# Optimization experiments

Measured on AMD Instinct MI355X. Metric: run time of the kernel, lower is better.

The kernel has to match this reference:

```python
import jax, jax.numpy as jnp
import numpy as np

N = 50000      # nodes
E = 800000     # edges (avg degree 16)
IN = 512       # input features
OUT = 32       # per-head hidden features
H = 8          # heads (layer 1)
C = 16         # classes (layer 2, 1 head)
NEG_SLOPE = 0.2


def setup_inputs() -> dict:
    key = jax.random.key(0)
    ks = jax.random.split(key, 8)
    x = jax.random.normal(ks[0], (N, IN), jnp.float32)
    edge_index = jax.random.randint(ks[1], (2, E), 0, N, jnp.int32)
    # layer 1 params: W1 [IN, H*OUT], attention vectors a1_src/a1_dst [H, OUT]
    W1 = jax.random.normal(ks[2], (IN, H * OUT), jnp.float32) * (1.0 / np.sqrt(IN))
    a1_src = jax.random.normal(ks[3], (H, OUT), jnp.float32) * (1.0 / np.sqrt(OUT))
    a1_dst = jax.random.normal(ks[4], (H, OUT), jnp.float32) * (1.0 / np.sqrt(OUT))
    # layer 2 params: single head, W2 [H*OUT, C], a2_src/a2_dst [1, C]
    W2 = jax.random.normal(ks[5], (H * OUT, C), jnp.float32) * (1.0 / np.sqrt(H * OUT))
    a2_src = jax.random.normal(ks[6], (1, C), jnp.float32) * (1.0 / np.sqrt(C))
    a2_dst = jax.random.normal(ks[7], (1, C), jnp.float32) * (1.0 / np.sqrt(C))
    return {"x": x, "W1": W1, "a1_src": a1_src, "a1_dst": a1_dst,
            "W2": W2, "a2_src": a2_src, "a2_dst": a2_dst,
            "edge_index": edge_index}


def gat_layer(x, edge_index, W, a_src, a_dst, concat):
    """Standard GAT layer: e_ij = LeakyReLU(a_src.Wh_i + a_dst.Wh_j),
    softmax over incoming edges of each target node, scatter-aggregate."""
    n = x.shape[0]
    h_heads, f = a_src.shape
    h = (x @ W).reshape(n, h_heads, f)                      # [N, H, F]
    src, dst = edge_index[0], edge_index[1]
    es = jnp.einsum('nhf,hf->nh', h, a_src)                 # [N, H] per-node src scores
    ed = jnp.einsum('nhf,hf->nh', h, a_dst)                 # [N, H]
    e = jax.nn.leaky_relu(es[src] + ed[dst], NEG_SLOPE)     # [E, H] per-edge logits
    # segment softmax over edges grouped by dst node
    m = jax.ops.segment_max(e, dst, num_segments=n)         # [N, H]
    m = jnp.where(jnp.isfinite(m), m, 0.0)                  # empty segments -> -inf
    p = jnp.exp(e - m[dst])                                 # [E, H]
    s = jax.ops.segment_sum(p, dst, num_segments=n)         # [N, H]
    denom = s[dst]
    alpha = p / jnp.where(denom > 0, denom, 1.0)            # [E, H]
    msg = h[src] * alpha[:, :, None]                        # [E, H, F]
    out = jax.ops.segment_sum(msg, dst, num_segments=n)     # [N, H, F]
    if concat:
        return out.reshape(n, h_heads * f)
    return out.mean(axis=1)


def reference(x, W1, a1_src, a1_dst, W2, a2_src, a2_dst, edge_index):
    # dropout is identity in eval mode
    h = gat_layer(x, edge_index, W1, a1_src, a1_dst, concat=True)   # [N, H*OUT]
    h = jax.nn.elu(h)
    h = gat_layer(h, edge_index, W2, a2_src, a2_dst, concat=False)  # [N, C]
    return jax.nn.log_softmax(h, axis=1)
```

## Files before the change

kernel.cpp:

```cpp
#include <hip/hip_runtime.h>

#define NN 50000
#define EE 800000
#define KIN 512
#define HF 256
#define NH 8
#define FOUT 32
#define NC 16
#define NEG 0.2f
#define NB_SCAN 196

typedef unsigned short u16;
typedef __attribute__((ext_vector_type(8))) short shortx8;
typedef __attribute__((ext_vector_type(4))) float floatx4;
typedef __attribute__((ext_vector_type(8))) unsigned short ushortx8;
typedef __attribute__((ext_vector_type(4))) unsigned short ushortx4;

__device__ __forceinline__ float lrelu(float x) { return x > 0.f ? x : NEG * x; }

__device__ __forceinline__ u16 f2bf(float f) {
    unsigned u = __float_as_uint(f);
    return (u16)((u + 0x7FFFu + ((u >> 16) & 1u)) >> 16);
}
__device__ __forceinline__ float bf2f(u16 v) {
    return __uint_as_float((unsigned)v << 16);
}

__device__ __forceinline__ void gll16(const void* g, void* l) {
    __builtin_amdgcn_global_load_lds((const __attribute__((address_space(1))) void*)g,
                                     (__attribute__((address_space(3))) void*)l, 16, 0, 0);
}

__global__ void count_deg(const int* __restrict__ dst, int* __restrict__ deg) {
    int e = blockIdx.x * 256 + threadIdx.x;
    if (e < EE) atomicAdd(&deg[dst[e]], 1);
}

__global__ __launch_bounds__(256) void scan_a(const int* __restrict__ deg, int* __restrict__ bsum) {
    __shared__ int sm[256];
    int t = threadIdx.x;
    int i = blockIdx.x * 256 + t;
    sm[t] = (i < NN) ? deg[i] : 0;
    __syncthreads();
    for (int o = 128; o; o >>= 1) { if (t < o) sm[t] += sm[t + o]; __syncthreads(); }
    if (t == 0) bsum[blockIdx.x] = sm[0];
}

__global__ __launch_bounds__(256) void scan_b(const int* __restrict__ bsum, int* __restrict__ boff) {
    __shared__ int sm[256];
    int t = threadIdx.x;
    sm[t] = (t < NB_SCAN) ? bsum[t] : 0;
    __syncthreads();
    for (int d = 1; d < 256; d <<= 1) {
        int v = (t >= d) ? sm[t - d] : 0;
        __syncthreads();
        sm[t] += v;
        __syncthreads();
    }
    if (t < NB_SCAN) boff[t] = (t == 0) ? 0 : sm[t - 1];
}

__global__ __launch_bounds__(256) void scan_c(const int* __restrict__ deg, const int* __restrict__ boff,
                                              int* __restrict__ off) {
    __shared__ int sm[256];
    int t = threadIdx.x;
    int i = blockIdx.x * 256 + t;
    int d = (i < NN) ? deg[i] : 0;
    sm[t] = d;
    __syncthreads();
    for (int dd = 1; dd < 256; dd <<= 1) {
        int v = (t >= dd) ? sm[t - dd] : 0;
        __syncthreads();
        sm[t] += v;
        __syncthreads();
    }
    if (i < NN) off[i] = boff[blockIdx.x] + sm[t] - d;
    if (i == 0) off[NN] = EE;
}

__global__ void fill_csr(const int* __restrict__ src, const int* __restrict__ dst,
                         const int* __restrict__ off, int* __restrict__ cursor,
                         int* __restrict__ csr_src) {
    int e = blockIdx.x * 256 + threadIdx.x;
    if (e < EE) {
        int d = dst[e];
        int pos = atomicAdd(&cursor[d], 1);
        csr_src[off[d] + pos] = src[e];
    }
}

__global__ __launch_bounds__(256) void convert_x(const float* __restrict__ x, u16* __restrict__ xb) {
    size_t i = ((size_t)blockIdx.x * 256 + threadIdx.x) * 8;
    if (i >= (size_t)NN * KIN) return;
    float4 f0 = *(const float4*)(x + i);
    float4 f1 = *(const float4*)(x + i + 4);
    ushortx8 o;
    o[0] = f2bf(f0.x); o[1] = f2bf(f0.y); o[2] = f2bf(f0.z); o[3] = f2bf(f0.w);
    o[4] = f2bf(f1.x); o[5] = f2bf(f1.y); o[6] = f2bf(f1.z); o[7] = f2bf(f1.w);
    *(ushortx8*)(xb + i) = o;
}

__global__ __launch_bounds__(256) void convert_w1t(const float* __restrict__ W1, u16* __restrict__ w1t) {
    int e = blockIdx.x * 256 + threadIdx.x;
    int k = e >> 8, n = e & 255;
    w1t[n * KIN + k] = f2bf(W1[e]);
}

__global__ __launch_bounds__(256) void convert_w2t(const float* __restrict__ W2, u16* __restrict__ w2t) {
    int e = blockIdx.x * 256 + threadIdx.x;
    int k = e >> 4, c = e & 15;
    w2t[c * HF + k] = f2bf(W2[e]);
}

__global__ __launch_bounds__(256) void gemm1_mfma(const u16* __restrict__ xb,
                                                  const u16* __restrict__ w1t,
                                                  u16* __restrict__ h1b) {
    __shared__ __align__(16) u16 As[128 * 32];
    __shared__ __align__(16) u16 Bs[128 * 32];
    int t = threadIdx.x;
    int lane = t & 63, wave = t >> 6;
    int wm = wave >> 1, wn = wave & 1;
    int lm = lane & 15, quad = lane >> 4;
    int bm = blockIdx.x * 128;
    int bn = blockIdx.y * 128;

    floatx4 acc[4][4];
#pragma unroll
    for (int i = 0; i < 4; i++)
#pragma unroll
        for (int j = 0; j < 4; j++) acc[i][j] = (floatx4){0.f, 0.f, 0.f, 0.f};

    int sr = wave * 32 + (lane >> 2);
    int sk = (lane & 3) * 8;
    int ar0 = bm + sr, ar1 = ar0 + 16;
    if (ar0 > NN - 1) ar0 = NN - 1;
    if (ar1 > NN - 1) ar1 = NN - 1;
    const u16* agp0 = xb + (size_t)ar0 * KIN + sk;
    const u16* agp1 = xb + (size_t)ar1 * KIN + sk;
    const u16* bgp0 = w1t + (size_t)(bn + sr) * KIN + sk;
    const u16* bgp1 = w1t + (size_t)(bn + sr + 16) * KIN + sk;
    u16* asl0 = As + wave * 1024;
    u16* asl1 = As + wave * 1024 + 512;
    u16* bsl0 = Bs + wave * 1024;
    u16* bsl1 = Bs + wave * 1024 + 512;

    int offA[4], offB[4];
#pragma unroll
    for (int i = 0; i < 4; i++) offA[i] = (wm * 64 + i * 16 + lm) * 32 + quad * 8;
#pragma unroll
    for (int j = 0; j < 4; j++) offB[j] = (wn * 64 + j * 16 + lm) * 32 + quad * 8;

    for (int kk = 0; kk < KIN; kk += 32) {
        gll16(agp0 + kk, asl0);
        gll16(agp1 + kk, asl1);
        gll16(bgp0 + kk, bsl0);
        gll16(bgp1 + kk, bsl1);
        __syncthreads();
        shortx8 af[4], bf[4];
#pragma unroll
        for (int i = 0; i < 4; i++) af[i] = *(const shortx8*)&As[offA[i]];
#pragma unroll
        for (int j = 0; j < 4; j++) bf[j] = *(const shortx8*)&Bs[offB[j]];
#pragma unroll
        for (int i = 0; i < 4; i++)
#pragma unroll
            for (int j = 0; j < 4; j++)
                acc[i][j] = __builtin_amdgcn_mfma_f32_16x16x32_bf16(af[i], bf[j], acc[i][j], 0, 0, 0);
        __syncthreads();
    }

#pragma unroll
    for (int i = 0; i < 4; i++) {
        int row = bm + wm * 64 + i * 16 + quad * 4;
#pragma unroll
        for (int j = 0; j < 4; j++) {
            int col = bn + wn * 64 + j * 16 + lm;
#pragma unroll
            for (int r = 0; r < 4; r++) {
                if (row + r < NN) h1b[(size_t)(row + r) * HF + col] = f2bf(acc[i][j][r]);
            }
        }
    }
}

__global__ __launch_bounds__(256) void scores1(const u16* __restrict__ h1b, const float* __restrict__ a_src,
                                               const float* __restrict__ a_dst,
                                               float* __restrict__ es, float* __restrict__ ed) {
    __shared__ float as_s[HF], ad_s[HF];
    int t = threadIdx.x;
    as_s[t] = a_src[t];
    ad_s[t] = a_dst[t];
    __syncthreads();
    int nl = t >> 5;
    int L = t & 31;
    int n = blockIdx.x * 8 + nl;
    ushortx8 hv = *(const ushortx8*)(h1b + (size_t)n * HF + L * 8);
    float ps = 0.f, pd = 0.f;
#pragma unroll
    for (int i = 0; i < 8; i++) {
        float v = bf2f(hv[i]);
        ps += v * as_s[L * 8 + i];
        pd += v * ad_s[L * 8 + i];
    }
    ps += __shfl_down(ps, 2, 4); ps += __shfl_down(ps, 1, 4);
    pd += __shfl_down(pd, 2, 4); pd += __shfl_down(pd, 1, 4);
    if ((L & 3) == 0) {
        int h = L >> 2;
        es[n * NH + h] = ps;
        ed[n * NH + h] = pd;
    }
}

__global__ __launch_bounds__(256) void agg1(const u16* __restrict__ h1b, const float* __restrict__ es,
                                            const float* __restrict__ ed, const int* __restrict__ off,
                                            const int* __restrict__ csr_src, u16* __restrict__ out1b) {
    int n = blockIdx.x, t = threadIdx.x;
    __shared__ float edl[NH];
    __shared__ float p_chunk[32][9];
    __shared__ float s_h[NH];
    __shared__ int src_chunk[32];
    __shared__ float red[4][HF];
    int beg = off[n];
    int deg = off[n + 1] - beg;
    if (t < NH) edl[t] = ed[n * NH + t];
    int ph = t >> 5, el = t & 31;
    int w = t >> 6, L = t & 63;
    int ah = L >> 3;
    float s_part = 0.f;
    float acc0 = 0.f, acc1 = 0.f, acc2 = 0.f, acc3 = 0.f;
    __syncthreads();
    float edh = edl[ph];
    for (int base = 0; base < deg; base += 32) {
        int nch = deg - base; if (nch > 32) nch = 32;
        if (t < nch) src_chunk[t] = csr_src[beg + base + t];
        __syncthreads();
        ushortx4 hv[8];
#pragma unroll
        for (int i = 0; i < 8; i++) {
            int e = w + i * 4;
            if (e < nch) hv[i] = *(const ushortx4*)(h1b + (size_t)src_chunk[e] * HF + L * 4);
        }
        float p = 0.f;
        if (el < nch) p = __expf(lrelu(es[src_chunk[el] * NH + ph] + edh));
        s_part += p;
        p_chunk[el][ph] = p;
        __syncthreads();
#pragma unroll
        for (int i = 0; i < 8; i++) {
            int e = w + i * 4;
            if (e < nch) {
                float p2 = p_chunk[e][ah];
                acc0 += p2 * bf2f(hv[i][0]);
                acc1 += p2 * bf2f(hv[i][1]);
                acc2 += p2 * bf2f(hv[i][2]);
                acc3 += p2 * bf2f(hv[i][3]);
            }
        }
        __syncthreads();
    }
#pragma unroll
    for (int o = 16; o; o >>= 1) s_part += __shfl_down(s_part, o, 32);
    if (el == 0) s_h[ph] = s_part;
    *(float4*)&red[w][L * 4] = make_float4(acc0, acc1, acc2, acc3);
    __syncthreads();
    float vv = red[0][t] + red[1][t] + red[2][t] + red[3][t];
    float sh = s_h[t >> 5];
    vv *= (sh > 0.f ? 1.0f / sh : 0.f);
    out1b[(size_t)n * HF + t] = f2bf(vv > 0.f ? vv : (__expf(vv) - 1.0f));
}

__global__ __launch_bounds__(64) void gemm2_mfma(const u16* __restrict__ out1b, const u16* __restrict__ w2t,
                                                 const float* __restrict__ a2s, const float* __restrict__ a2d,
                                                 float* __restrict__ h2, float* __restrict__ es2,
                                                 float* __restrict__ ed2) {
    int lane = threadIdx.x;
    int lm = lane & 15, quad = lane >> 4;
    int nb = blockIdx.x * 16;
    floatx4 acc = (floatx4){0.f, 0.f, 0.f, 0.f};
    const u16* arow = out1b + (size_t)(nb + lm) * HF + quad * 8;
    const u16* brow = w2t + lm * HF + quad * 8;
#pragma unroll
    for (int kk = 0; kk < HF; kk += 32) {
        shortx8 af = *(const shortx8*)(arow + kk);
        shortx8 bf = *(const shortx8*)(brow + kk);
        acc = __builtin_amdgcn_mfma_f32_16x16x32_bf16(af, bf, acc, 0, 0, 0);
    }
    float a2sc = a2s[lm], a2dc = a2d[lm];
#pragma unroll
    for (int r = 0; r < 4; r++) {
        int n = nb + quad * 4 + r;
        float v = acc[r];
        h2[n * NC + lm] = v;
        float ps = v * a2sc, pd = v * a2dc;
#pragma unroll
        for (int o = 8; o; o >>= 1) {
            ps += __shfl_down(ps, o, 16);
            pd += __shfl_down(pd, o, 16);
        }
        if (lm == 0) { es2[n] = ps; ed2[n] = pd; }
    }
}

__global__ __launch_bounds__(256) void agg2(const float* __restrict__ h2, const float* __restrict__ es2,
                                            const float* __restrict__ ed2, const int* __restrict__ off,
                                            const int* __restrict__ csr_src, float* __restrict__ out) {
    int t = threadIdx.x;
    int nid = blockIdx.x * 16 + (t >> 4);
    int c = t & 15;
    int beg = off[nid];
    int deg = off[nid + 1] - beg;
    float edn = ed2[nid];
    float s = 0.f, acc = 0.f;
    for (int base = 0; base < deg; base += 16) {
        int nch = deg - base; if (nch > 16) nch = 16;
        int sv = 0;
        if (c < nch) sv = csr_src[beg + base + c];
        int sva[16];
#pragma unroll
        for (int e = 0; e < 16; e++) sva[e] = __shfl(sv, e, 16);
        float hva[16];
#pragma unroll
        for (int e = 0; e < 16; e++) hva[e] = h2[sva[e] * NC + c];
        float p = 0.f;
        if (c < nch) p = __expf(lrelu(es2[sv] + edn));
        s += p;
        float pa[16];
#pragma unroll
        for (int e = 0; e < 16; e++) pa[e] = __shfl(p, e, 16);
#pragma unroll
        for (int e = 0; e < 16; e++) acc += pa[e] * hva[e];
    }
#pragma unroll
    for (int o = 8; o; o >>= 1) s += __shfl_down(s, o, 16);
    s = __shfl(s, 0, 16);
    float v = (s > 0.f) ? acc / s : 0.f;
    float m2 = v;
#pragma unroll
    for (int o = 8; o; o >>= 1) m2 = fmaxf(m2, __shfl_down(m2, o, 16));
    m2 = __shfl(m2, 0, 16);
    float se = __expf(v - m2);
#pragma unroll
    for (int o = 8; o; o >>= 1) se += __shfl_down(se, o, 16);
    se = __shfl(se, 0, 16);
    out[nid * NC + c] = v - m2 - __logf(se);
}

extern "C" void kernel_launch(void* const* d_in, const int* in_sizes, int n_in,
                              void* d_out, int out_size, void* d_ws, size_t ws_size,
                              hipStream_t stream) {
    const float* x   = (const float*)d_in[0];
    const float* W1  = (const float*)d_in[1];
    const float* a1s = (const float*)d_in[2];
    const float* a1d = (const float*)d_in[3];
    const float* W2  = (const float*)d_in[4];
    const float* a2s = (const float*)d_in[5];
    const float* a2d = (const float*)d_in[6];
    const int*   ei  = (const int*)d_in[7];
    const int* srcv = ei;
    const int* dstv = ei + EE;
    float* out = (float*)d_out;

    u16* h1b   = (u16*)d_ws;
    u16* xb    = h1b + (size_t)NN * HF;
    u16* out1b = xb;
    float* es1 = (float*)(xb + (size_t)NN * KIN);
    float* ed1 = es1 + (size_t)NN * NH;
    float* h2  = ed1 + (size_t)NN * NH;
    u16* w1t   = (u16*)h2;
    float* es2v = h2 + (size_t)NN * NC;
    float* ed2v = es2v + NN;
    int* deg    = (int*)(ed2v + NN);
    int* cursor = deg + NN;
    int* offs   = cursor + NN;
    int* csr    = offs + NN + 1;
    int* bsum   = csr + EE;
    int* boff   = bsum + 256;
    u16* w2t    = (u16*)(boff + 256);

    hipMemsetAsync(deg, 0, NN * sizeof(int), stream);
    hipMemsetAsync(cursor, 0, NN * sizeof(int), stream);
    count_deg<<<(EE + 255) / 256, 256, 0, stream>>>(dstv, deg);
    scan_a<<<NB_SCAN, 256, 0, stream>>>(deg, bsum);
    scan_b<<<1, 256, 0, stream>>>(bsum, boff);
    scan_c<<<NB_SCAN, 256, 0, stream>>>(deg, boff, offs);
    fill_csr<<<(EE + 255) / 256, 256, 0, stream>>>(srcv, dstv, offs, cursor, csr);
    convert_x<<<((size_t)NN * KIN / 8 + 255) / 256, 256, 0, stream>>>(x, xb);
    convert_w1t<<<(KIN * HF) / 256, 256, 0, stream>>>(W1, w1t);
    convert_w2t<<<(HF * NC) / 256, 256, 0, stream>>>(W2, w2t);
    gemm1_mfma<<<dim3((NN + 127) / 128, HF / 128), 256, 0, stream>>>(xb, w1t, h1b);
    scores1<<<NN / 8, 256, 0, stream>>>(h1b, a1s, a1d, es1, ed1);
    agg1<<<NN, 256, 0, stream>>>(h1b, es1, ed1, offs, csr, out1b);
    gemm2_mfma<<<NN / 16, 64, 0, stream>>>(out1b, w2t, a2s, a2d, h2, es2v, ed2v);
    agg2<<<NN / 16, 256, 0, stream>>>(h2, es2v, ed2v, offs, csr, out);
}
```

Baseline: 424.6 us.

## Fuse fp32-to-bf16 x conversion into GEMM1, widen N tile, wave-per-node aggregation

GEMM1 now loads fp32 x directly into LDS and converts to bf16 while building fragments. This removes the separate convert_x pass and its 50000x512 bf16 round trip through memory. Each block now covers all 256 output columns, so x is read once instead of twice, at the cost of more accumulator registers and more LDS. agg1 is rewritten to process one node per wave with no __syncthreads and vectorized 16-byte feature loads. The weight conversions and the two memsets are each merged into one launch.

```diff
diff --git a/kernel.cpp b/kernel.cpp
--- a/kernel.cpp
+++ b/kernel.cpp
@@ -14,7 +14,7 @@
 typedef __attribute__((ext_vector_type(8))) short shortx8;
 typedef __attribute__((ext_vector_type(4))) float floatx4;
 typedef __attribute__((ext_vector_type(8))) unsigned short ushortx8;
-typedef __attribute__((ext_vector_type(4))) unsigned short ushortx4;
+typedef __attribute__((ext_vector_type(4))) unsigned uintx4;
 
 __device__ __forceinline__ float lrelu(float x) { return x > 0.f ? x : NEG * x; }
 
@@ -24,6 +24,10 @@
 }
 __device__ __forceinline__ float bf2f(u16 v) {
     return __uint_as_float((unsigned)v << 16);
+}
+__device__ __forceinline__ unsigned pk2bf(float a, float b) {
+    unsigned ua = __float_as_uint(a), ub = __float_as_uint(b);
+    return ((ua + 0x8000u) >> 16) | ((ub + 0x8000u) & 0xffff0000u);
 }
 
 __device__ __forceinline__ void gll16(const void* g, void* l) {
@@ -89,82 +93,90 @@
     }
 }
 
-__global__ __launch_bounds__(256) void convert_x(const float* __restrict__ x, u16* __restrict__ xb) {
-    size_t i = ((size_t)blockIdx.x * 256 + threadIdx.x) * 8;
-    if (i >= (size_t)NN * KIN) return;
-    float4 f0 = *(const float4*)(x + i);
-    float4 f1 = *(const float4*)(x + i + 4);
-    ushortx8 o;
-    o[0] = f2bf(f0.x); o[1] = f2bf(f0.y); o[2] = f2bf(f0.z); o[3] = f2bf(f0.w);
-    o[4] = f2bf(f1.x); o[5] = f2bf(f1.y); o[6] = f2bf(f1.z); o[7] = f2bf(f1.w);
-    *(ushortx8*)(xb + i) = o;
-}
-
-__global__ __launch_bounds__(256) void convert_w1t(const float* __restrict__ W1, u16* __restrict__ w1t) {
+__global__ __launch_bounds__(256) void convert_w(const float* __restrict__ W1, const float* __restrict__ W2,
+                                                 u16* __restrict__ w1t, u16* __restrict__ w2t) {
     int e = blockIdx.x * 256 + threadIdx.x;
-    int k = e >> 8, n = e & 255;
-    w1t[n * KIN + k] = f2bf(W1[e]);
-}
-
-__global__ __launch_bounds__(256) void convert_w2t(const float* __restrict__ W2, u16* __restrict__ w2t) {
-    int e = blockIdx.x * 256 + threadIdx.x;
-    int k = e >> 4, c = e & 15;
-    w2t[c * HF + k] = f2bf(W2[e]);
-}
-
-__global__ __launch_bounds__(256) void gemm1_mfma(const u16* __restrict__ xb,
-                                                  const u16* __restrict__ w1t,
-                                                  u16* __restrict__ h1b) {
-    __shared__ __align__(16) u16 As[128 * 32];
-    __shared__ __align__(16) u16 Bs[128 * 32];
+    if (e < KIN * HF) {
+        int k = e >> 8, n = e & 255;
+        w1t[n * KIN + k] = f2bf(W1[e]);
+    } else {
+        int e2 = e - KIN * HF;
+        if (e2 < HF * NC) {
+            int k = e2 >> 4, c = e2 & 15;
+            w2t[c * HF + k] = f2bf(W2[e2]);
+        }
+    }
+}
+
+__global__ __launch_bounds__(256, 2) void gemm1_mfma(const float* __restrict__ x,
+                                                     const u16* __restrict__ w1t,
+                                                     u16* __restrict__ h1b) {
+    __shared__ __align__(16) float As[128 * 32];
+    __shared__ __align__(16) u16 Bs[256 * 32];
     int t = threadIdx.x;
     int lane = t & 63, wave = t >> 6;
     int wm = wave >> 1, wn = wave & 1;
     int lm = lane & 15, quad = lane >> 4;
     int bm = blockIdx.x * 128;
-    int bn = blockIdx.y * 128;
-
-    floatx4 acc[4][4];
+
+    floatx4 acc[4][8];
 #pragma unroll
     for (int i = 0; i < 4; i++)
 #pragma unroll
-        for (int j = 0; j < 4; j++) acc[i][j] = (floatx4){0.f, 0.f, 0.f, 0.f};
-
-    int sr = wave * 32 + (lane >> 2);
-    int sk = (lane & 3) * 8;
-    int ar0 = bm + sr, ar1 = ar0 + 16;
-    if (ar0 > NN - 1) ar0 = NN - 1;
-    if (ar1 > NN - 1) ar1 = NN - 1;
-    const u16* agp0 = xb + (size_t)ar0 * KIN + sk;
-    const u16* agp1 = xb + (size_t)ar1 * KIN + sk;
-    const u16* bgp0 = w1t + (size_t)(bn + sr) * KIN + sk;
-    const u16* bgp1 = w1t + (size_t)(bn + sr + 16) * KIN + sk;
-    u16* asl0 = As + wave * 1024;
-    u16* asl1 = As + wave * 1024 + 512;
-    u16* bsl0 = Bs + wave * 1024;
-    u16* bsl1 = Bs + wave * 1024 + 512;
-
-    int offA[4], offB[4];
+        for (int j = 0; j < 8; j++) acc[i][j] = (floatx4){0.f, 0.f, 0.f, 0.f};
+
+    int arow_l = wave * 32 + (lane >> 3);
+    int akoff = (lane & 7) * 4;
+    const float* aptr[4];
+#pragma unroll
+    for (int i = 0; i < 4; i++) {
+        int ar = bm + arow_l + i * 8;
+        if (ar > NN - 1) ar = NN - 1;
+        aptr[i] = x + (size_t)ar * KIN + akoff;
+    }
+    float* alds[4];
+#pragma unroll
+    for (int i = 0; i < 4; i++) alds[i] = As + (wave * 32 + i * 8) * 32;
+
+    int brow_l = wave * 64 + (lane >> 2);
+    int bkoff = (lane & 3) * 8;
+    const u16* bptr[4];
+#pragma unroll
+    for (int i = 0; i < 4; i++) bptr[i] = w1t + (size_t)(brow_l + i * 16) * KIN + bkoff;
+    u16* blds[4];
+#pragma unroll
+    for (int i = 0; i < 4; i++) blds[i] = Bs + (wave * 64 + i * 16) * 32;
+
+    int offA[4], offB[8];
 #pragma unroll
     for (int i = 0; i < 4; i++) offA[i] = (wm * 64 + i * 16 + lm) * 32 + quad * 8;
 #pragma unroll
-    for (int j = 0; j < 4; j++) offB[j] = (wn * 64 + j * 16 + lm) * 32 + quad * 8;
+    for (int j = 0; j < 8; j++) offB[j] = (wn * 128 + j * 16 + lm) * 32 + quad * 8;
 
     for (int kk = 0; kk < KIN; kk += 32) {
-        gll16(agp0 + kk, asl0);
-        gll16(agp1 + kk, asl1);
-        gll16(bgp0 + kk, bsl0);
-        gll16(bgp1 + kk, bsl1);
-        __syncthreads();
-        shortx8 af[4], bf[4];
-#pragma unroll
-        for (int i = 0; i < 4; i++) af[i] = *(const shortx8*)&As[offA[i]];
-#pragma unroll
-        for (int j = 0; j < 4; j++) bf[j] = *(const shortx8*)&Bs[offB[j]];
+#pragma unroll
+        for (int i = 0; i < 4; i++) gll16(aptr[i] + kk, alds[i]);
+#pragma unroll
+        for (int i = 0; i < 4; i++) gll16(bptr[i] + kk, blds[i]);
+        __syncthreads();
+        shortx8 af[4], bf[8];
+#pragma unroll
+        for (int i = 0; i < 4; i++) {
+            const float4* ap = (const float4*)&As[offA[i]];
+            float4 lo = ap[0], hi = ap[1];
+            union { uintx4 u; shortx8 s; } cv;
+            cv.u[0] = pk2bf(lo.x, lo.y);
+            cv.u[1] = pk2bf(lo.z, lo.w);
+            cv.u[2] = pk2bf(hi.x, hi.y);
+            cv.u[3] = pk2bf(hi.z, hi.w);
+            af[i] = cv.s;
+        }
+#pragma unroll
+        for (int j = 0; j < 8; j++) bf[j] = *(const shortx8*)&Bs[offB[j]];
 #pragma unroll
         for (int i = 0; i < 4; i++)
 #pragma unroll
-            for (int j = 0; j < 4; j++)
+            for (int j = 0; j < 8; j++)
                 acc[i][j] = __builtin_amdgcn_mfma_f32_16x16x32_bf16(af[i], bf[j], acc[i][j], 0, 0, 0);
         __syncthreads();
     }
@@ -173,8 +185,8 @@
     for (int i = 0; i < 4; i++) {
         int row = bm + wm * 64 + i * 16 + quad * 4;
 #pragma unroll
-        for (int j = 0; j < 4; j++) {
-            int col = bn + wn * 64 + j * 16 + lm;
+        for (int j = 0; j < 8; j++) {
+            int col = wn * 128 + j * 16 + lm;
 #pragma unroll
             for (int r = 0; r < 4; r++) {
                 if (row + r < NN) h1b[(size_t)(row + r) * HF + col] = f2bf(acc[i][j][r]);
@@ -214,59 +226,50 @@
 __global__ __launch_bounds__(256) void agg1(const u16* __restrict__ h1b, const float* __restrict__ es,
                                             const float* __restrict__ ed, const int* __restrict__ off,
                                             const int* __restrict__ csr_src, u16* __restrict__ out1b) {
-    int n = blockIdx.x, t = threadIdx.x;
-    __shared__ float edl[NH];
-    __shared__ float p_chunk[32][9];
-    __shared__ float s_h[NH];
-    __shared__ int src_chunk[32];
-    __shared__ float red[4][HF];
+    int wave = threadIdx.x >> 6;
+    int lane = threadIdx.x & 63;
+    int n = blockIdx.x * 4 + wave;
+    int fh = lane & 31;
+    int ep = lane >> 5;
+    int head = fh >> 2;
     int beg = off[n];
     int deg = off[n + 1] - beg;
-    if (t < NH) edl[t] = ed[n * NH + t];
-    int ph = t >> 5, el = t & 31;
-    int w = t >> 6, L = t & 63;
-    int ah = L >> 3;
+    float edh = ed[n * NH + head];
+    const u16* hbase = h1b + fh * 8;
+    float acc[8] = {0.f, 0.f, 0.f, 0.f, 0.f, 0.f, 0.f, 0.f};
     float s_part = 0.f;
-    float acc0 = 0.f, acc1 = 0.f, acc2 = 0.f, acc3 = 0.f;
-    __syncthreads();
-    float edh = edl[ph];
-    for (int base = 0; base < deg; base += 32) {
-        int nch = deg - base; if (nch > 32) nch = 32;
-        if (t < nch) src_chunk[t] = csr_src[beg + base + t];
-        __syncthreads();
-        ushortx4 hv[8];
-#pragma unroll
-        for (int i = 0; i < 8; i++) {
-            int e = w + i * 4;
-            if (e < nch) hv[i] = *(const ushortx4*)(h1b + (size_t)src_chunk[e] * HF + L * 4);
-        }
-        float p = 0.f;
-        if (el < nch) p = __expf(lrelu(es[src_chunk[el] * NH + ph] + edh));
-        s_part += p;
-        p_chunk[el][ph] = p;
-        __syncthreads();
-#pragma unroll
-        for (int i = 0; i < 8; i++) {
-            int e = w + i * 4;
-            if (e < nch) {
-                float p2 = p_chunk[e][ah];
-                acc0 += p2 * bf2f(hv[i][0]);
-                acc1 += p2 * bf2f(hv[i][1]);
-                acc2 += p2 * bf2f(hv[i][2]);
-                acc3 += p2 * bf2f(hv[i][3]);
+    for (int base = 0; base < deg; base += 16) {
+        int nch = deg - base; if (nch > 16) nch = 16;
+        int sv = (lane < nch) ? csr_src[beg + base + lane] : 0;
+#pragma unroll
+        for (int e = 0; e < 8; e++) {
+            int ee = 2 * e + ep;
+            int s = __shfl(sv, ee, 64);
+            if (ee < nch) {
+                float lg = es[s * NH + head] + edh;
+                float p = __expf(lg > 0.f ? lg : NEG * lg);
+                ushortx8 hv = *(const ushortx8*)(hbase + (size_t)s * HF);
+                s_part += p;
+#pragma unroll
+                for (int i = 0; i < 8; i++) acc[i] += p * bf2f(hv[i]);
             }
         }
-        __syncthreads();
-    }
-#pragma unroll
-    for (int o = 16; o; o >>= 1) s_part += __shfl_down(s_part, o, 32);
-    if (el == 0) s_h[ph] = s_part;
-    *(float4*)&red[w][L * 4] = make_float4(acc0, acc1, acc2, acc3);
-    __syncthreads();
-    float vv = red[0][t] + red[1][t] + red[2][t] + red[3][t];
-    float sh = s_h[t >> 5];
-    vv *= (sh > 0.f ? 1.0f / sh : 0.f);
-    out1b[(size_t)n * HF + t] = f2bf(vv > 0.f ? vv : (__expf(vv) - 1.0f));
+    }
+#pragma unroll
+    for (int i = 0; i < 8; i++) acc[i] += __shfl_down(acc[i], 32, 64);
+    s_part += __shfl_down(s_part, 32, 64);
+    if (lane < 32) {
+        float inv = s_part > 0.f ? 1.0f / s_part : 0.f;
+        union { uintx4 u; ushortx8 v; } ob;
+#pragma unroll
+        for (int i = 0; i < 4; i++) {
+            float v0 = acc[2 * i] * inv, v1 = acc[2 * i + 1] * inv;
+            v0 = v0 > 0.f ? v0 : (__expf(v0) - 1.0f);
+            v1 = v1 > 0.f ? v1 : (__expf(v1) - 1.0f);
+            ob.u[i] = (unsigned)f2bf(v0) | ((unsigned)f2bf(v1) << 16);
+        }
+        *(ushortx8*)(out1b + (size_t)n * HF + fh * 8) = ob.v;
+    }
 }
 
 __global__ __launch_bounds__(64) void gemm2_mfma(const u16* __restrict__ out1b, const u16* __restrict__ w2t,
@@ -360,13 +363,11 @@
     const int* dstv = ei + EE;
     float* out = (float*)d_out;
 
-    u16* h1b   = (u16*)d_ws;
-    u16* xb    = h1b + (size_t)NN * HF;
-    u16* out1b = xb;
-    float* es1 = (float*)(xb + (size_t)NN * KIN);
-    float* ed1 = es1 + (size_t)NN * NH;
-    float* h2  = ed1 + (size_t)NN * NH;
-    u16* w1t   = (u16*)h2;
+    u16* h1b    = (u16*)d_ws;
+    u16* out1b  = h1b + (size_t)NN * HF;
+    float* es1  = (float*)(out1b + (size_t)NN * HF);
+    float* ed1  = es1 + (size_t)NN * NH;
+    float* h2   = ed1 + (size_t)NN * NH;
     float* es2v = h2 + (size_t)NN * NC;
     float* ed2v = es2v + NN;
     int* deg    = (int*)(ed2v + NN);
@@ -375,21 +376,19 @@
     int* csr    = offs + NN + 1;
     int* bsum   = csr + EE;
     int* boff   = bsum + 256;
-    u16* w2t    = (u16*)(boff + 256);
-
-    hipMemsetAsync(deg, 0, NN * sizeof(int), stream);
-    hipMemsetAsync(cursor, 0, NN * sizeof(int), stream);
+    u16* w1t    = (u16*)(boff + 256);
+    u16* w2t    = w1t + (size_t)HF * KIN;
+
+    hipMemsetAsync(deg, 0, 2 * NN * sizeof(int), stream);
     count_deg<<<(EE + 255) / 256, 256, 0, stream>>>(dstv, deg);
     scan_a<<<NB_SCAN, 256, 0, stream>>>(deg, bsum);
     scan_b<<<1, 256, 0, stream>>>(bsum, boff);
     scan_c<<<NB_SCAN, 256, 0, stream>>>(deg, boff, offs);
     fill_csr<<<(EE + 255) / 256, 256, 0, stream>>>(srcv, dstv, offs, cursor, csr);
-    convert_x<<<((size_t)NN * KIN / 8 + 255) / 256, 256, 0, stream>>>(x, xb);
-    convert_w1t<<<(KIN * HF) / 256, 256, 0, stream>>>(W1, w1t);
-    convert_w2t<<<(HF * NC) / 256, 256, 0, stream>>>(W2, w2t);
-    gemm1_mfma<<<dim3((NN + 127) / 128, HF / 128), 256, 0, stream>>>(xb, w1t, h1b);
+    convert_w<<<(KIN * HF + HF * NC + 255) / 256, 256, 0, stream>>>(W1, W2, w1t, w2t);
+    gemm1_mfma<<<(NN + 127) / 128, 256, 0, stream>>>(x, w1t, h1b);
     scores1<<<NN / 8, 256, 0, stream>>>(h1b, a1s, a1d, es1, ed1);
-    agg1<<<NN, 256, 0, stream>>>(h1b, es1, ed1, offs, csr, out1b);
+    agg1<<<NN / 4, 256, 0, stream>>>(h1b, es1, ed1, offs, csr, out1b);
     gemm2_mfma<<<NN / 16, 64, 0, stream>>>(out1b, w2t, a2s, a2d, h2, es2v, ed2v);
     agg2<<<NN / 16, 256, 0, stream>>>(h2, es2v, ed2v, offs, csr, out);
 }
```

Measured after the change: 360.7 us. 15.0% less time.
